# Performance work log

Hardware: AMD Instinct MI355X
Metric: run time of the kernel (lower is better)

Reference implementation:

```python
import jax, jax.numpy as jnp
import numpy as np

NUM_CLASSES = 10
TAU = 3.3333333


def thermometer_encode(x, thresholds):
    # x: [B, F], thresholds: [F, T] -> binary bits [B, F*T]
    bits = (x[:, :, None] > thresholds[None, :, :]).astype(x.dtype)
    B = x.shape[0]
    return bits.reshape(B, -1)


def lut_layer(h, idx, luts):
    # h: [B, I] activations in [0,1]; idx: [O, n] input mapping; luts: [O, 2^n]
    # Multilinear interpolation over the 2^n LUT corners (gather + fold).
    xs = h[:, idx]                       # [B, O, n] gathered inputs
    B, O, n = xs.shape
    acc = jnp.broadcast_to(luts[None, :, :], (B, O, luts.shape[1]))  # [B, O, 2^n]
    for k in range(n):                   # fold one input bit per step (MSB first)
        half = acc.shape[-1] // 2
        xk = xs[:, :, k:k + 1]           # [B, O, 1]
        acc = acc[..., :half] * (1.0 - xk) + acc[..., half:] * xk
    return acc[..., 0]                   # [B, O]


def group_sum(h, k, tau):
    # h: [B, W] -> [B, k] popcount-style grouped sum scaled by 1/tau
    B, W = h.shape
    return h.reshape(B, k, W // k).sum(axis=-1) / tau


def setup_inputs() -> dict:
    key = jax.random.key(0)
    ks = jax.random.split(key, 6)
    B, F, T = 512, 1024, 3
    I = F * T                            # 3072 thermometer bits
    O1, O2, n = 2000, 1000, 6
    x = jax.random.normal(ks[0], (B, F), dtype=jnp.float32)
    thresholds = jax.random.normal(ks[1], (F, T), dtype=jnp.float32)
    luts1 = jax.random.uniform(ks[2], (O1, 2 ** n), dtype=jnp.float32)
    idx1 = jax.random.randint(ks[3], (O1, n), 0, I, dtype=jnp.int32)
    luts2 = jax.random.uniform(ks[4], (O2, 2 ** n), dtype=jnp.float32)
    idx2 = jax.random.randint(ks[5], (O2, n), 0, O1, dtype=jnp.int32)
    return {"x": x, "thresholds": thresholds, "luts1": luts1, "idx1": idx1,
            "luts2": luts2, "idx2": idx2}


def reference(x, thresholds, luts1, idx1, luts2, idx2):
    h = thermometer_encode(x, thresholds)     # [B, 3072] binary
    h = lut_layer(h, idx1, luts1)             # [B, 2000]
    h = lut_layer(h, idx2, luts2)             # [B, 1000]
    return group_sum(h, NUM_CLASSES, TAU)     # [B, 10]
```

## Files before the change

kernel.cpp:

```cpp
#include <hip/hip_runtime.h>


#define FEAT  1024
#define O1    2000
#define O2    1000
#define NCLS  10

#define WS_BITS_OFF  0
#define WS_H1_OFF    (256 << 10)
#define WS_H2_OFF    ((256 << 10) + (4 << 20))

__global__ __launch_bounds__(512) void k1_thermo_pack(
    const float* __restrict__ x,
    const float* __restrict__ thr,
    unsigned long long* __restrict__ bitsT)
{
    const int r    = threadIdx.x;
    const int w    = r >> 6;
    const int lane = r & 63;
    const int f0   = blockIdx.x * 4;

    float4 xv4 = *(const float4*)(x + (size_t)r * FEAT + f0);
    float xa[4] = {xv4.x, xv4.y, xv4.z, xv4.w};

#pragma unroll
    for (int f = 0; f < 4; ++f) {
        const float* tp = thr + (size_t)(f0 + f) * 3;
#pragma unroll
        for (int j = 0; j < 3; ++j) {
            unsigned long long m = __ballot(xa[f] > tp[j]);
            if (lane == 0)
                bitsT[(size_t)((f0 + f) * 3 + j) * 8 + w] = m;
        }
    }
}

__global__ __launch_bounds__(512) void k2_layer1(
    const int*   __restrict__ idx1,
    const float* __restrict__ luts1,
    const unsigned long long* __restrict__ bitsT,
    float* __restrict__ h1T)
{
    const int o    = blockIdx.x;
    const int r    = threadIdx.x;
    const int w    = r >> 6;
    const int lane = r & 63;
    const int* ip  = idx1 + o * 6;

    unsigned long long m0 = bitsT[(size_t)ip[0] * 8 + w];
    unsigned long long m1 = bitsT[(size_t)ip[1] * 8 + w];
    unsigned long long m2 = bitsT[(size_t)ip[2] * 8 + w];
    unsigned long long m3 = bitsT[(size_t)ip[3] * 8 + w];
    unsigned long long m4 = bitsT[(size_t)ip[4] * 8 + w];
    unsigned long long m5 = bitsT[(size_t)ip[5] * 8 + w];

    int code = ((int)((m0 >> lane) & 1ull) << 5)
             | ((int)((m1 >> lane) & 1ull) << 4)
             | ((int)((m2 >> lane) & 1ull) << 3)
             | ((int)((m3 >> lane) & 1ull) << 2)
             | ((int)((m4 >> lane) & 1ull) << 1)
             |  (int)((m5 >> lane) & 1ull);

    h1T[(size_t)o * 512 + r] = luts1[o * 64 + code];
}

__global__ __launch_bounds__(512) void k3_layer2(
    const int*   __restrict__ idx2,
    const float* __restrict__ luts2,
    const float* __restrict__ h1T,
    float* __restrict__ h2T)
{
    const int o   = blockIdx.x;
    const int r   = threadIdx.x;
    const int* ip = idx2 + o * 6;

    float xv0 = h1T[(size_t)ip[0] * 512 + r];
    float xv1 = h1T[(size_t)ip[1] * 512 + r];
    float xv2 = h1T[(size_t)ip[2] * 512 + r];
    float xv3 = h1T[(size_t)ip[3] * 512 + r];
    float xv4 = h1T[(size_t)ip[4] * 512 + r];
    float xv5 = h1T[(size_t)ip[5] * 512 + r];

    const float4* lp = (const float4*)(luts2 + (size_t)o * 64);
    float v[16];
#pragma unroll
    for (int q = 0; q < 16; ++q) {
        float4 e = lp[q];
        float u0 = e.x + xv5 * (e.y - e.x);
        float u1 = e.z + xv5 * (e.w - e.z);
        v[q] = u0 + xv4 * (u1 - u0);
    }
#pragma unroll
    for (int q = 0; q < 8; ++q) v[q] = v[2*q] + xv3 * (v[2*q+1] - v[2*q]);
#pragma unroll
    for (int q = 0; q < 4; ++q) v[q] = v[2*q] + xv2 * (v[2*q+1] - v[2*q]);
#pragma unroll
    for (int q = 0; q < 2; ++q) v[q] = v[2*q] + xv1 * (v[2*q+1] - v[2*q]);
    h2T[(size_t)o * 512 + r] = v[0] + xv0 * (v[1] - v[0]);
}

__global__ __launch_bounds__(256) void k4_reduce(
    const float* __restrict__ h2T,
    float* __restrict__ out)
{
    const int c = blockIdx.x >> 1;
    const int r = ((blockIdx.x & 1) << 8) | threadIdx.x;
    const float* hp = h2T + (size_t)c * 100 * 512 + r;

    float s = 0.0f;
#pragma unroll
    for (int p = 0; p < 10; ++p) {
        float s2 = 0.0f;
#pragma unroll
        for (int j = 0; j < 10; ++j) s2 += hp[(size_t)(p * 10 + j) * 512];
        s += s2;
    }
    out[r * NCLS + c] = s / 3.3333333f;
}

extern "C" void kernel_launch(void* const* d_in, const int* in_sizes, int n_in,
                              void* d_out, int out_size, void* d_ws, size_t ws_size,
                              hipStream_t stream) {
    const float* x     = (const float*)d_in[0];
    const float* thr   = (const float*)d_in[1];
    const float* luts1 = (const float*)d_in[2];
    const int*   idx1  = (const int*)  d_in[3];
    const float* luts2 = (const float*)d_in[4];
    const int*   idx2  = (const int*)  d_in[5];
    float* out = (float*)d_out;

    char* ws = (char*)d_ws;
    unsigned long long* bitsT = (unsigned long long*)(ws + WS_BITS_OFF);
    float* h1T = (float*)(ws + WS_H1_OFF);
    float* h2T = (float*)(ws + WS_H2_OFF);

    k1_thermo_pack<<<FEAT / 4, 512, 0, stream>>>(x, thr, bitsT);
    k2_layer1<<<O1, 512, 0, stream>>>(idx1, luts1, bitsT, h1T);
    k3_layer2<<<O2, 512, 0, stream>>>(idx2, luts2, h1T, h2T);
    k4_reduce<<<NCLS * 2, 256, 0, stream>>>(h2T, out);
}
```

Measured before the change: 82.33 us.

## Fuse four stage kernels into one persistent kernel with software grid barriers

Merges thermometer packing, both LUT layers and the group-sum reduction into a single persistent kernel of 256 blocks by 1024 threads. Per-stage kernel launches are replaced by an atomic-counter grid barrier, and work is spread across waves with grid-stride task loops. This removes launch and drain gaps between the small stages. In exchange it adds barrier spin cost and relies on all blocks being co-resident; otherwise the barrier could deadlock or time out.

```diff
diff --git a/kernel.cpp b/kernel.cpp
--- a/kernel.cpp
+++ b/kernel.cpp
@@ -1,121 +1,148 @@
 #include <hip/hip_runtime.h>
 
 
-#define FEAT  1024
-#define O1    2000
-#define O2    1000
-#define NCLS  10
+#define FEAT   1024
+#define O1     2000
+#define O2     1000
+#define NCLS   10
+#define NB     256
+#define NT     1024
+#define NWAVES (NB * (NT / 64))
 
 #define WS_BITS_OFF  0
 #define WS_H1_OFF    (256 << 10)
 #define WS_H2_OFF    ((256 << 10) + (4 << 20))
 
-__global__ __launch_bounds__(512) void k1_thermo_pack(
+__device__ unsigned g_bar_cnt = 0;
+__device__ unsigned g_bar_gen = 0;
+
+__device__ __forceinline__ void grid_barrier() {
+    __syncthreads();
+    if (threadIdx.x == 0) {
+        const unsigned gen =
+            __hip_atomic_load(&g_bar_gen, __ATOMIC_RELAXED, __HIP_MEMORY_SCOPE_AGENT);
+        const unsigned n =
+            __hip_atomic_fetch_add(&g_bar_cnt, 1u, __ATOMIC_ACQ_REL, __HIP_MEMORY_SCOPE_AGENT);
+        if (n + 1u == (unsigned)gridDim.x) {
+            __hip_atomic_store(&g_bar_cnt, 0u, __ATOMIC_RELAXED, __HIP_MEMORY_SCOPE_AGENT);
+            __hip_atomic_fetch_add(&g_bar_gen, 1u, __ATOMIC_ACQ_REL, __HIP_MEMORY_SCOPE_AGENT);
+        } else {
+            for (int spin = 0; spin < (1 << 22); ++spin) {
+                if (__hip_atomic_load(&g_bar_gen, __ATOMIC_ACQUIRE,
+                                      __HIP_MEMORY_SCOPE_AGENT) != gen) break;
+                __builtin_amdgcn_s_sleep(2);
+            }
+        }
+    }
+    __syncthreads();
+}
+
+__global__ __launch_bounds__(NT, 4) void dwn_onekernel(
     const float* __restrict__ x,
     const float* __restrict__ thr,
-    unsigned long long* __restrict__ bitsT)
+    const float* __restrict__ luts1,
+    const int*   __restrict__ idx1,
+    const float* __restrict__ luts2,
+    const int*   __restrict__ idx2,
+    float* __restrict__ out,
+    unsigned long long* __restrict__ bitsT,
+    float* __restrict__ h1T,
+    float* __restrict__ h2T)
 {
-    const int r    = threadIdx.x;
-    const int w    = r >> 6;
-    const int lane = r & 63;
-    const int f0   = blockIdx.x * 4;
+    const int t    = threadIdx.x;
+    const int lane = t & 63;
+    const int wl   = t >> 6;
+    const int b    = blockIdx.x;
+    const int gw   = (b << 4) | wl;
 
-    float4 xv4 = *(const float4*)(x + (size_t)r * FEAT + f0);
-    float xa[4] = {xv4.x, xv4.y, xv4.z, xv4.w};
-
+    {
+        const int w8    = wl & 7;
+        const int row   = (w8 << 6) | lane;
+        const int fbase = (b << 2) | ((wl >> 3) << 1);
 #pragma unroll
-    for (int f = 0; f < 4; ++f) {
-        const float* tp = thr + (size_t)(f0 + f) * 3;
+        for (int ff = 0; ff < 2; ++ff) {
+            const int f = fbase + ff;
+            const float xv = x[(size_t)row * FEAT + f];
+            const float* tp = thr + (size_t)f * 3;
 #pragma unroll
-        for (int j = 0; j < 3; ++j) {
-            unsigned long long m = __ballot(xa[f] > tp[j]);
-            if (lane == 0)
-                bitsT[(size_t)((f0 + f) * 3 + j) * 8 + w] = m;
+            for (int j = 0; j < 3; ++j) {
+                unsigned long long m = __ballot(xv > tp[j]);
+                if (lane == 0)
+                    bitsT[(size_t)(f * 3 + j) * 8 + w8] = m;
+            }
         }
     }
-}
+    grid_barrier();
 
-__global__ __launch_bounds__(512) void k2_layer1(
-    const int*   __restrict__ idx1,
-    const float* __restrict__ luts1,
-    const unsigned long long* __restrict__ bitsT,
-    float* __restrict__ h1T)
-{
-    const int o    = blockIdx.x;
-    const int r    = threadIdx.x;
-    const int w    = r >> 6;
-    const int lane = r & 63;
-    const int* ip  = idx1 + o * 6;
+    for (int task = gw; task < O1 * 8; task += NWAVES) {
+        const int o = task >> 3;
+        const int w = task & 7;
+        const int* ip = idx1 + o * 6;
 
-    unsigned long long m0 = bitsT[(size_t)ip[0] * 8 + w];
-    unsigned long long m1 = bitsT[(size_t)ip[1] * 8 + w];
-    unsigned long long m2 = bitsT[(size_t)ip[2] * 8 + w];
-    unsigned long long m3 = bitsT[(size_t)ip[3] * 8 + w];
-    unsigned long long m4 = bitsT[(size_t)ip[4] * 8 + w];
-    unsigned long long m5 = bitsT[(size_t)ip[5] * 8 + w];
+        const unsigned long long m0 = bitsT[(size_t)ip[0] * 8 + w];
+        const unsigned long long m1 = bitsT[(size_t)ip[1] * 8 + w];
+        const unsigned long long m2 = bitsT[(size_t)ip[2] * 8 + w];
+        const unsigned long long m3 = bitsT[(size_t)ip[3] * 8 + w];
+        const unsigned long long m4 = bitsT[(size_t)ip[4] * 8 + w];
+        const unsigned long long m5 = bitsT[(size_t)ip[5] * 8 + w];
 
-    int code = ((int)((m0 >> lane) & 1ull) << 5)
-             | ((int)((m1 >> lane) & 1ull) << 4)
-             | ((int)((m2 >> lane) & 1ull) << 3)
-             | ((int)((m3 >> lane) & 1ull) << 2)
-             | ((int)((m4 >> lane) & 1ull) << 1)
-             |  (int)((m5 >> lane) & 1ull);
+        const int code = ((int)((m0 >> lane) & 1ull) << 5)
+                       | ((int)((m1 >> lane) & 1ull) << 4)
+                       | ((int)((m2 >> lane) & 1ull) << 3)
+                       | ((int)((m3 >> lane) & 1ull) << 2)
+                       | ((int)((m4 >> lane) & 1ull) << 1)
+                       |  (int)((m5 >> lane) & 1ull);
 
-    h1T[(size_t)o * 512 + r] = luts1[o * 64 + code];
-}
+        h1T[(size_t)o * 512 + (w << 6) + lane] = luts1[o * 64 + code];
+    }
+    grid_barrier();
 
-__global__ __launch_bounds__(512) void k3_layer2(
-    const int*   __restrict__ idx2,
-    const float* __restrict__ luts2,
-    const float* __restrict__ h1T,
-    float* __restrict__ h2T)
-{
-    const int o   = blockIdx.x;
-    const int r   = threadIdx.x;
-    const int* ip = idx2 + o * 6;
+    for (int task = gw; task < O2 * 8; task += NWAVES) {
+        const int o  = task >> 3;
+        const int rr = ((task & 7) << 6) | lane;
+        const int* ip = idx2 + o * 6;
 
-    float xv0 = h1T[(size_t)ip[0] * 512 + r];
-    float xv1 = h1T[(size_t)ip[1] * 512 + r];
-    float xv2 = h1T[(size_t)ip[2] * 512 + r];
-    float xv3 = h1T[(size_t)ip[3] * 512 + r];
-    float xv4 = h1T[(size_t)ip[4] * 512 + r];
-    float xv5 = h1T[(size_t)ip[5] * 512 + r];
+        const float xv0 = h1T[(size_t)ip[0] * 512 + rr];
+        const float xv1 = h1T[(size_t)ip[1] * 512 + rr];
+        const float xv2 = h1T[(size_t)ip[2] * 512 + rr];
+        const float xv3 = h1T[(size_t)ip[3] * 512 + rr];
+        const float xv4 = h1T[(size_t)ip[4] * 512 + rr];
+        const float xv5 = h1T[(size_t)ip[5] * 512 + rr];
 
-    const float4* lp = (const float4*)(luts2 + (size_t)o * 64);
-    float v[16];
+        const float4* lp = (const float4*)(luts2 + (size_t)o * 64);
+        float v[16];
 #pragma unroll
-    for (int q = 0; q < 16; ++q) {
-        float4 e = lp[q];
-        float u0 = e.x + xv5 * (e.y - e.x);
-        float u1 = e.z + xv5 * (e.w - e.z);
-        v[q] = u0 + xv4 * (u1 - u0);
+        for (int q = 0; q < 16; ++q) {
+            float4 e = lp[q];
+            float u0 = e.x + xv5 * (e.y - e.x);
+            float u1 = e.z + xv5 * (e.w - e.z);
+            v[q] = u0 + xv4 * (u1 - u0);
+        }
+#pragma unroll
+        for (int q = 0; q < 8; ++q) v[q] = v[2*q] + xv3 * (v[2*q+1] - v[2*q]);
+#pragma unroll
+        for (int q = 0; q < 4; ++q) v[q] = v[2*q] + xv2 * (v[2*q+1] - v[2*q]);
+#pragma unroll
+        for (int q = 0; q < 2; ++q) v[q] = v[2*q] + xv1 * (v[2*q+1] - v[2*q]);
+        h2T[(size_t)o * 512 + rr] = v[0] + xv0 * (v[1] - v[0]);
     }
+    grid_barrier();
+
+    if (gw < NCLS * 8) {
+        const int c  = gw >> 3;
+        const int rr = ((gw & 7) << 6) | lane;
+        const float* hp = h2T + (size_t)c * 100 * 512 + rr;
+
+        float s = 0.0f;
 #pragma unroll
-    for (int q = 0; q < 8; ++q) v[q] = v[2*q] + xv3 * (v[2*q+1] - v[2*q]);
+        for (int p = 0; p < 10; ++p) {
+            float s2 = 0.0f;
 #pragma unroll
-    for (int q = 0; q < 4; ++q) v[q] = v[2*q] + xv2 * (v[2*q+1] - v[2*q]);
-#pragma unroll
-    for (int q = 0; q < 2; ++q) v[q] = v[2*q] + xv1 * (v[2*q+1] - v[2*q]);
-    h2T[(size_t)o * 512 + r] = v[0] + xv0 * (v[1] - v[0]);
-}
-
-__global__ __launch_bounds__(256) void k4_reduce(
-    const float* __restrict__ h2T,
-    float* __restrict__ out)
-{
-    const int c = blockIdx.x >> 1;
-    const int r = ((blockIdx.x & 1) << 8) | threadIdx.x;
-    const float* hp = h2T + (size_t)c * 100 * 512 + r;
-
-    float s = 0.0f;
-#pragma unroll
-    for (int p = 0; p < 10; ++p) {
-        float s2 = 0.0f;
-#pragma unroll
-        for (int j = 0; j < 10; ++j) s2 += hp[(size_t)(p * 10 + j) * 512];
-        s += s2;
+            for (int j = 0; j < 10; ++j) s2 += hp[(size_t)(p * 10 + j) * 512];
+            s += s2;
+        }
+        out[rr * NCLS + c] = s / 3.3333333f;
     }
-    out[r * NCLS + c] = s / 3.3333333f;
 }
 
 extern "C" void kernel_launch(void* const* d_in, const int* in_sizes, int n_in,
@@ -134,8 +161,6 @@
     float* h1T = (float*)(ws + WS_H1_OFF);
     float* h2T = (float*)(ws + WS_H2_OFF);
 
-    k1_thermo_pack<<<FEAT / 4, 512, 0, stream>>>(x, thr, bitsT);
-    k2_layer1<<<O1, 512, 0, stream>>>(idx1, luts1, bitsT, h1T);
-    k3_layer2<<<O2, 512, 0, stream>>>(idx2, luts2, h1T, h2T);
-    k4_reduce<<<NCLS * 2, 256, 0, stream>>>(h2T, out);
+    dwn_onekernel<<<NB, NT, 0, stream>>>(x, thr, luts1, idx1, luts2, idx2,
+                                         out, bitsT, h1T, h2T);
 }
```

After: 172.8 us. 2.1x slower.

## Fuse all stages into one persistent kernel with flag-based grid sync

Applied to the files above, without the earlier changes.

Replaces the four kernel launches with one kernel of 512 blocks. Each block recomputes the layer-1 LUT outputs it needs directly from x and the thresholds, so the packed bit buffer and the h1 intermediate are no longer materialised. Layer-2 results are written with relaxed atomics, and the first ten blocks spin on per-block release flags before doing the class reduction. This removes launch overhead and intermediate memory traffic. In exchange it recomputes each layer-1 value several times, relies on all 512 blocks being co-resident, and puts a spin-wait at the end.

```diff
diff --git a/kernel.cpp b/kernel.cpp
--- a/kernel.cpp
+++ b/kernel.cpp
@@ -5,117 +5,125 @@
 #define O1    2000
 #define O2    1000
 #define NCLS  10
+#define NB    512
+#define NT    512
 
-#define WS_BITS_OFF  0
-#define WS_H1_OFF    (256 << 10)
-#define WS_H2_OFF    ((256 << 10) + (4 << 20))
+#define SCOPE_AGENT __HIP_MEMORY_SCOPE_AGENT
 
-__global__ __launch_bounds__(512) void k1_thermo_pack(
+__device__ unsigned g_flags[NB];
+
+__device__ __forceinline__ float h1_compute(
+    const float* __restrict__ x, const float* __restrict__ thr,
+    const float* __restrict__ luts1, const int* __restrict__ idx1,
+    int o1, int r)
+{
+    const int2* ip = (const int2*)(idx1 + o1 * 6);
+    const int2 q0 = ip[0], q1 = ip[1], q2 = ip[2];
+    const float* xr = x + (size_t)r * FEAT;
+    const int b0 = xr[q0.x / 3] > thr[q0.x];
+    const int b1 = xr[q0.y / 3] > thr[q0.y];
+    const int b2 = xr[q1.x / 3] > thr[q1.x];
+    const int b3 = xr[q1.y / 3] > thr[q1.y];
+    const int b4 = xr[q2.x / 3] > thr[q2.x];
+    const int b5 = xr[q2.y / 3] > thr[q2.y];
+    const int code = (b0 << 5) | (b1 << 4) | (b2 << 3)
+                   | (b3 << 2) | (b4 << 1) | b5;
+    return luts1[o1 * 64 + code];
+}
+
+__global__ __launch_bounds__(NT, 4) void dwn_ob(
     const float* __restrict__ x,
     const float* __restrict__ thr,
-    unsigned long long* __restrict__ bitsT)
+    const float* __restrict__ luts1,
+    const int*   __restrict__ idx1,
+    const float* __restrict__ luts2,
+    const int*   __restrict__ idx2,
+    float* __restrict__ out,
+    float* __restrict__ h2T)
 {
-    const int r    = threadIdx.x;
-    const int w    = r >> 6;
-    const int lane = r & 63;
-    const int f0   = blockIdx.x * 4;
+    const int t = threadIdx.x;
+    const int b = blockIdx.x;
 
-    float4 xv4 = *(const float4*)(x + (size_t)r * FEAT + f0);
-    float xa[4] = {xv4.x, xv4.y, xv4.z, xv4.w};
+    const unsigned base =
+        __hip_atomic_load(&g_flags[b], __ATOMIC_RELAXED, SCOPE_AGENT);
 
 #pragma unroll
-    for (int f = 0; f < 4; ++f) {
-        const float* tp = thr + (size_t)(f0 + f) * 3;
+    for (int k = 0; k < 2; ++k) {
+        const int o2 = b + k * NB;
+        if (o2 < O2) {
+            const int2* ip = (const int2*)(idx2 + o2 * 6);
+            const int2 p0 = ip[0], p1 = ip[1], p2 = ip[2];
+            const float xv0 = h1_compute(x, thr, luts1, idx1, p0.x, t);
+            const float xv1 = h1_compute(x, thr, luts1, idx1, p0.y, t);
+            const float xv2 = h1_compute(x, thr, luts1, idx1, p1.x, t);
+            const float xv3 = h1_compute(x, thr, luts1, idx1, p1.y, t);
+            const float xv4 = h1_compute(x, thr, luts1, idx1, p2.x, t);
+            const float xv5 = h1_compute(x, thr, luts1, idx1, p2.y, t);
+
+            const float4* lp = (const float4*)(luts2 + (size_t)o2 * 64);
+            float v[16];
 #pragma unroll
-        for (int j = 0; j < 3; ++j) {
-            unsigned long long m = __ballot(xa[f] > tp[j]);
-            if (lane == 0)
-                bitsT[(size_t)((f0 + f) * 3 + j) * 8 + w] = m;
+            for (int q = 0; q < 16; ++q) {
+                float4 e = lp[q];
+                float u0 = e.x + xv5 * (e.y - e.x);
+                float u1 = e.z + xv5 * (e.w - e.z);
+                v[q] = u0 + xv4 * (u1 - u0);
+            }
+#pragma unroll
+            for (int q = 0; q < 8; ++q) v[q] = v[2*q] + xv3 * (v[2*q+1] - v[2*q]);
+#pragma unroll
+            for (int q = 0; q < 4; ++q) v[q] = v[2*q] + xv2 * (v[2*q+1] - v[2*q]);
+#pragma unroll
+            for (int q = 0; q < 2; ++q) v[q] = v[2*q] + xv1 * (v[2*q+1] - v[2*q]);
+            const float h2 = v[0] + xv0 * (v[1] - v[0]);
+
+            __hip_atomic_store(&h2T[(size_t)o2 * 512 + t], h2,
+                               __ATOMIC_RELAXED, SCOPE_AGENT);
         }
     }
-}
 
-__global__ __launch_bounds__(512) void k2_layer1(
-    const int*   __restrict__ idx1,
-    const float* __restrict__ luts1,
-    const unsigned long long* __restrict__ bitsT,
-    float* __restrict__ h1T)
-{
-    const int o    = blockIdx.x;
-    const int r    = threadIdx.x;
-    const int w    = r >> 6;
-    const int lane = r & 63;
-    const int* ip  = idx1 + o * 6;
+    __syncthreads();
+    if (t == 0)
+        __hip_atomic_store(&g_flags[b], base + 1u, __ATOMIC_RELEASE, SCOPE_AGENT);
 
-    unsigned long long m0 = bitsT[(size_t)ip[0] * 8 + w];
-    unsigned long long m1 = bitsT[(size_t)ip[1] * 8 + w];
-    unsigned long long m2 = bitsT[(size_t)ip[2] * 8 + w];
-    unsigned long long m3 = bitsT[(size_t)ip[3] * 8 + w];
-    unsigned long long m4 = bitsT[(size_t)ip[4] * 8 + w];
-    unsigned long long m5 = bitsT[(size_t)ip[5] * 8 + w];
+    if (b >= NCLS) return;
 
-    int code = ((int)((m0 >> lane) & 1ull) << 5)
-             | ((int)((m1 >> lane) & 1ull) << 4)
-             | ((int)((m2 >> lane) & 1ull) << 3)
-             | ((int)((m3 >> lane) & 1ull) << 2)
-             | ((int)((m4 >> lane) & 1ull) << 1)
-             |  (int)((m5 >> lane) & 1ull);
+    {
+        const unsigned target = base + 1u;
+        if (t < 64) {
+            for (int spin = 0; spin < (1 << 18); ++spin) {
+                bool ok = true;
+#pragma unroll
+                for (int kk = 0; kk < NB / 64; ++kk) {
+                    unsigned v = __hip_atomic_load(&g_flags[t + 64 * kk],
+                                                   __ATOMIC_RELAXED, SCOPE_AGENT);
+                    ok &= (v >= target);
+                }
+                if (__all(ok)) break;
+                __builtin_amdgcn_s_sleep(8);
+            }
+            __builtin_amdgcn_fence(__ATOMIC_ACQUIRE, "agent");
+        }
+        __syncthreads();
+    }
 
-    h1T[(size_t)o * 512 + r] = luts1[o * 64 + code];
-}
-
-__global__ __launch_bounds__(512) void k3_layer2(
-    const int*   __restrict__ idx2,
-    const float* __restrict__ luts2,
-    const float* __restrict__ h1T,
-    float* __restrict__ h2T)
-{
-    const int o   = blockIdx.x;
-    const int r   = threadIdx.x;
-    const int* ip = idx2 + o * 6;
-
-    float xv0 = h1T[(size_t)ip[0] * 512 + r];
-    float xv1 = h1T[(size_t)ip[1] * 512 + r];
-    float xv2 = h1T[(size_t)ip[2] * 512 + r];
-    float xv3 = h1T[(size_t)ip[3] * 512 + r];
-    float xv4 = h1T[(size_t)ip[4] * 512 + r];
-    float xv5 = h1T[(size_t)ip[5] * 512 + r];
-
-    const float4* lp = (const float4*)(luts2 + (size_t)o * 64);
-    float v[16];
+    {
+        const int c = b;
+        float s = 0.0f;
 #pragma unroll
-    for (int q = 0; q < 16; ++q) {
-        float4 e = lp[q];
-        float u0 = e.x + xv5 * (e.y - e.x);
-        float u1 = e.z + xv5 * (e.w - e.z);
-        v[q] = u0 + xv4 * (u1 - u0);
+        for (int p = 0; p < 10; ++p) {
+            float s2 = 0.0f;
+#pragma unroll
+            for (int j = 0; j < 10; ++j) {
+                const float hv = __hip_atomic_load(
+                    &h2T[(size_t)(c * 100 + p * 10 + j) * 512 + t],
+                    __ATOMIC_RELAXED, SCOPE_AGENT);
+                s2 += hv;
+            }
+            s += s2;
+        }
+        out[t * NCLS + c] = s / 3.3333333f;
     }
-#pragma unroll
-    for (int q = 0; q < 8; ++q) v[q] = v[2*q] + xv3 * (v[2*q+1] - v[2*q]);
-#pragma unroll
-    for (int q = 0; q < 4; ++q) v[q] = v[2*q] + xv2 * (v[2*q+1] - v[2*q]);
-#pragma unroll
-    for (int q = 0; q < 2; ++q) v[q] = v[2*q] + xv1 * (v[2*q+1] - v[2*q]);
-    h2T[(size_t)o * 512 + r] = v[0] + xv0 * (v[1] - v[0]);
-}
-
-__global__ __launch_bounds__(256) void k4_reduce(
-    const float* __restrict__ h2T,
-    float* __restrict__ out)
-{
-    const int c = blockIdx.x >> 1;
-    const int r = ((blockIdx.x & 1) << 8) | threadIdx.x;
-    const float* hp = h2T + (size_t)c * 100 * 512 + r;
-
-    float s = 0.0f;
-#pragma unroll
-    for (int p = 0; p < 10; ++p) {
-        float s2 = 0.0f;
-#pragma unroll
-        for (int j = 0; j < 10; ++j) s2 += hp[(size_t)(p * 10 + j) * 512];
-        s += s2;
-    }
-    out[r * NCLS + c] = s / 3.3333333f;
 }
 
 extern "C" void kernel_launch(void* const* d_in, const int* in_sizes, int n_in,
@@ -128,14 +136,7 @@
     const float* luts2 = (const float*)d_in[4];
     const int*   idx2  = (const int*)  d_in[5];
     float* out = (float*)d_out;
+    float* h2T = (float*)d_ws;
 
-    char* ws = (char*)d_ws;
-    unsigned long long* bitsT = (unsigned long long*)(ws + WS_BITS_OFF);
-    float* h1T = (float*)(ws + WS_H1_OFF);
-    float* h2T = (float*)(ws + WS_H2_OFF);
-
-    k1_thermo_pack<<<FEAT / 4, 512, 0, stream>>>(x, thr, bitsT);
-    k2_layer1<<<O1, 512, 0, stream>>>(idx1, luts1, bitsT, h1T);
-    k3_layer2<<<O2, 512, 0, stream>>>(idx2, luts2, h1T, h2T);
-    k4_reduce<<<NCLS * 2, 256, 0, stream>>>(h2T, out);
+    dwn_ob<<<NB, NT, 0, stream>>>(x, thr, luts1, idx1, luts2, idx2, out, h2T);
 }
```

Result: slower. 149.1 us (+81.1%).
